# Kernel tuning notes

Hardware: AMD Instinct MI355X
Metric: run time of the kernel (lower is better)

Reference implementation:

```python
import jax, jax.numpy as jnp
import numpy as np

N_NODES = 50000
N_GRAPHS = 64


def gcn_conv(x, W, b, row, col, norm, n):
    # PyG GCNConv: h = x @ W; out[i] = sum_{(j,i) in E+selfloops} norm_ji * h[j] + b
    h = x @ W
    msg = norm[:, None] * h[row]
    out = jax.ops.segment_sum(msg, col, num_segments=n)
    return out + b


def setup_inputs() -> dict:
    key = jax.random.key(0)
    ks = jax.random.split(key, 12)
    F_in, H, C = 128, 128, 16
    x = jax.random.normal(ks[0], (N_NODES, F_in), dtype=jnp.float32)
    edge_index = jax.random.randint(ks[1], (2, 800000), 0, N_NODES, dtype=jnp.int64)
    batch = jnp.sort(jax.random.randint(ks[2], (N_NODES,), 0, N_GRAPHS, dtype=jnp.int64))
    def glorot(k, shape):
        lim = np.sqrt(6.0 / (shape[0] + shape[1]))
        return jax.random.uniform(k, shape, jnp.float32, -lim, lim)
    return {
        "x": x,
        "edge_index": edge_index,
        "batch": batch,
        "W0": glorot(ks[3], (F_in, H)), "b0": jnp.zeros((H,), jnp.float32),
        "W1": glorot(ks[4], (H, H)),   "b1": jnp.zeros((H,), jnp.float32),
        "W2": glorot(ks[5], (H, H)),   "b2": jnp.zeros((H,), jnp.float32),
        "lin_W": glorot(ks[6], (H, C)),
        "lin_b": jnp.zeros((C,), jnp.float32),
    }


def reference(x, edge_index, batch, W0, b0, W1, b1, W2, b2, lin_W, lin_b):
    n = x.shape[0]
    # add self-loops
    loops = jnp.arange(n, dtype=edge_index.dtype)
    row = jnp.concatenate([edge_index[0], loops])
    col = jnp.concatenate([edge_index[1], loops])
    # symmetric normalization: deg over destination (col) incl. self-loops
    deg = jax.ops.segment_sum(jnp.ones_like(col, dtype=x.dtype), col, num_segments=n)
    dinv = jnp.where(deg > 0, jax.lax.rsqrt(deg), 0.0)
    norm = dinv[row] * dinv[col]

    h = gcn_conv(x, W0, b0, row, col, norm, n)
    h = jax.nn.relu(h)
    h = gcn_conv(h, W1, b1, row, col, norm, n)
    h = jax.nn.relu(h)
    h = gcn_conv(h, W2, b2, row, col, norm, n)

    # global mean pool over graphs
    sums = jax.ops.segment_sum(h, batch, num_segments=N_GRAPHS)
    cnts = jax.ops.segment_sum(jnp.ones((n,), h.dtype), batch, num_segments=N_GRAPHS)
    pooled = sums / jnp.maximum(cnts, 1.0)[:, None]

    # dropout is identity in eval mode
    logits = pooled @ lin_W + lin_b
    return jax.nn.softmax(logits, axis=1)
```

## Files before the change

kernel.cpp:

```cpp
#include <hip/hip_runtime.h>


#define NF 128
#define MAXBUCK 512
#define CAP 2560
#define L1_CHUNK 8192
#define L1_THREADS 512
#define L1_PER_THREAD 16
#define PPG 8

typedef __attribute__((ext_vector_type(8))) short short8;
typedef __attribute__((ext_vector_type(4))) float floatx4;
typedef __attribute__((ext_vector_type(2))) float floatx2;

__device__ __forceinline__ unsigned int bf16_rne(float x) {
    unsigned int u = __float_as_uint(x);
    return (u + 0x7fffu + ((u >> 16) & 1u)) >> 16;
}
__device__ __forceinline__ unsigned int pack_bf16_rne(float x, float y) {
    return bf16_rne(x) | (bf16_rne(y) << 16);
}

__global__ __launch_bounds__(256) void k_repack_w3(const float* __restrict__ W0,
                                                   const float* __restrict__ W1,
                                                   const float* __restrict__ W2,
                                                   unsigned short* __restrict__ whi,
                                                   unsigned short* __restrict__ wlo,
                                                   int* __restrict__ bucket_cursor) {
    if (blockIdx.x == 0) {
        for (int i = threadIdx.x; i <= MAXBUCK; i += 256) bucket_cursor[i] = 0;
    }
    int wsel = blockIdx.x >> 3;
    const float* W = (wsel == 0) ? W0 : (wsel == 1) ? W1 : W2;
    int idx = (blockIdx.x & 7) * 256 + threadIdx.x;
    int slab = wsel * NF * NF;
    int l = idx & 63;
    int t = (idx >> 6) & 7;
    int s = idx >> 9;
    int kbase = s * 32 + (l >> 4) * 8;
    int nn = t * 16 + (l & 15);
    #pragma unroll
    for (int j = 0; j < 8; ++j) {
        float w = W[(kbase + j) * NF + nn];
        unsigned int h = bf16_rne(w);
        float hf = __uint_as_float(h << 16);
        unsigned int lo = bf16_rne(w - hf);
        whi[slab + idx * 8 + j] = (unsigned short)h;
        wlo[slab + idx * 8 + j] = (unsigned short)lo;
    }
}

__global__ __launch_bounds__(L1_THREADS) void k_bucket_scatter(
        const int* __restrict__ row, const int* __restrict__ colv,
        int* __restrict__ bucket_cursor, unsigned int* __restrict__ buck_arr,
        int ne, int etot, int nbuck) {
    __shared__ unsigned int hist[MAXBUCK];
    __shared__ unsigned int lbase[MAXBUCK];
    __shared__ unsigned int lcur[MAXBUCK];
    __shared__ unsigned int runb[MAXBUCK];
    __shared__ unsigned int sa[MAXBUCK], sb[MAXBUCK];
    __shared__ unsigned int reorder[L1_CHUNK];
    int t = threadIdx.x;
    int e0 = blockIdx.x * L1_CHUNK;
    int cnt_here = min(etot - e0, L1_CHUNK);

    hist[t] = 0;
    __syncthreads();

    unsigned int myv[L1_PER_THREAD];
    #pragma unroll
    for (int j = 0; j < L1_PER_THREAD; ++j) {
        int e = e0 + j * L1_THREADS + t;
        if (e < etot) {
            int s, d;
            if (e < ne) { s = row[e]; d = colv[e]; } else { s = d = e - ne; }
            myv[j] = (unsigned int)s | ((unsigned int)d << 16);
            atomicAdd(&hist[d >> 7], 1u);
        } else myv[j] = 0xffffffffu;
    }
    __syncthreads();

    sa[t] = hist[t];
    __syncthreads();
    unsigned int* pin = sa;
    unsigned int* pout = sb;
    #pragma unroll
    for (int off = 1; off < MAXBUCK; off <<= 1) {
        pout[t] = pin[t] + ((t >= off) ? pin[t - off] : 0);
        __syncthreads();
        unsigned int* tmp = pin; pin = pout; pout = tmp;
    }
    unsigned int ex = pin[t] - hist[t];
    lbase[t] = ex;
    lcur[t]  = ex;
    if (t < nbuck && hist[t] > 0)
        runb[t] = (unsigned int)atomicAdd(&bucket_cursor[t], (int)hist[t]);
    __syncthreads();

    #pragma unroll
    for (int j = 0; j < L1_PER_THREAD; ++j) {
        unsigned int v = myv[j];
        if (v != 0xffffffffu) {
            unsigned int p = atomicAdd(&lcur[v >> 23], 1u);
            reorder[p] = v;
        }
    }
    __syncthreads();

    for (int i = t; i < cnt_here; i += L1_THREADS) {
        unsigned int v = reorder[i];
        unsigned int b = v >> 23;
        buck_arr[(size_t)b * CAP + runb[b] + ((unsigned int)i - lbase[b])] = v;
    }
}

__global__ __launch_bounds__(256) void k_fine(const unsigned int* __restrict__ buck_arr,
                                              const int* __restrict__ bucket_cursor,
                                              int* __restrict__ starts,
                                              int* __restrict__ ends,
                                              float* __restrict__ dinv,
                                              unsigned short* __restrict__ src16,
                                              int n) {
    int b = blockIdx.x;
    int base = b * CAP;
    int m = min(bucket_cursor[b], CAP);
    int node0 = b << 7;
    int nn = min(128, n - node0);
    __shared__ unsigned int cnt[128];
    __shared__ unsigned int lsc[256];
    __shared__ unsigned int lcur[128];
    __shared__ unsigned short srcbuf[CAP];
    int t = threadIdx.x;
    if (t < 128) cnt[t] = 0;
    __syncthreads();
    for (int i = t; i < m; i += 256)
        atomicAdd(&cnt[(buck_arr[base + i] >> 16) - node0], 1u);
    __syncthreads();
    unsigned int v0 = (t < 128) ? cnt[t] : 0;
    lsc[t] = v0;
    __syncthreads();
    #pragma unroll
    for (int off = 1; off < 128; off <<= 1) {
        unsigned int add = (t >= off) ? lsc[t - off] : 0;
        __syncthreads();
        lsc[t] += add;
        __syncthreads();
    }
    if (t < 128) {
        unsigned int ex = lsc[t] - v0;
        lcur[t] = ex;
        if (t < nn) {
            starts[node0 + t] = base + (int)ex;
            ends[node0 + t]   = base + (int)(ex + v0);
            dinv[node0 + t]   = rsqrtf((float)v0);
        }
    }
    __syncthreads();
    for (int i = t; i < m; i += 256) {
        unsigned int v = buck_arr[base + i];
        unsigned int p = atomicAdd(&lcur[(v >> 16) - node0], 1u);
        srcbuf[p] = (unsigned short)(v & 0xffffu);
    }
    __syncthreads();
    for (int i = t; i < m; i += 256)
        src16[base + i] = srcbuf[i];
}

__global__ __launch_bounds__(256) void k_gemm_mfma(const float* __restrict__ Af,
                                                   const unsigned short* __restrict__ Ab,
                                                   const unsigned short* __restrict__ Whi,
                                                   const unsigned short* __restrict__ Wlo,
                                                   const float* __restrict__ dinv,
                                                   unsigned char* __restrict__ Out,
                                                   int M) {
    __shared__ unsigned short As[64 * 136];
    int tid = threadIdx.x;
    int row0 = blockIdx.x * 64;

    if (Af) {
        for (int c = tid; c < 1024; c += 256) {
            int r = c >> 4, off = c & 15;
            int gr = min(row0 + r, M - 1);
            const float4* p = (const float4*)(Af + (size_t)gr * NF) + off * 2;
            float4 v0 = p[0], v1 = p[1];
            uint4 pk;
            pk.x = pack_bf16_rne(v0.x, v0.y);
            pk.y = pack_bf16_rne(v0.z, v0.w);
            pk.z = pack_bf16_rne(v1.x, v1.y);
            pk.w = pack_bf16_rne(v1.z, v1.w);
            *(uint4*)(&As[r * 136 + off * 8]) = pk;
        }
    } else {
        for (int c = tid; c < 1024; c += 256) {
            int r = c >> 4, off = c & 15;
            int gr = min(row0 + r, M - 1);
            *(uint4*)(&As[r * 136 + off * 8]) = ((const uint4*)(Ab + (size_t)gr * NF))[off];
        }
    }
    __syncthreads();

    int wave = tid >> 6, l = tid & 63;
    int q = l >> 4, c16 = l & 15;
    int wrow0 = wave * 16;

    floatx4 acc[8];
    #pragma unroll
    for (int t = 0; t < 8; ++t) acc[t] = (floatx4){0.f, 0.f, 0.f, 0.f};

    #pragma unroll
    for (int s = 0; s < 4; ++s) {
        short8 a = *(const short8*)(&As[(wrow0 + c16) * 136 + s * 32 + q * 8]);
        #pragma unroll
        for (int t = 0; t < 8; ++t) {
            short8 bh = *(const short8*)(Whi + ((size_t)((s * 8 + t) * 64 + l) * 8));
            acc[t] = __builtin_amdgcn_mfma_f32_16x16x32_bf16(a, bh, acc[t], 0, 0, 0);
            short8 bl = *(const short8*)(Wlo + ((size_t)((s * 8 + t) * 64 + l) * 8));
            acc[t] = __builtin_amdgcn_mfma_f32_16x16x32_bf16(a, bl, acc[t], 0, 0, 0);
        }
    }

    float ds[4];
    #pragma unroll
    for (int i = 0; i < 4; ++i) {
        int gr = row0 + wrow0 + q * 4 + i;
        ds[i] = (gr < M) ? dinv[gr] : 0.f;
    }
    #pragma unroll
    for (int t = 0; t < 8; ++t) {
        #pragma unroll
        for (int i = 0; i < 4; ++i) {
            int gr = row0 + wrow0 + q * 4 + i;
            if (gr < M) {
                float v = acc[t][i] * ds[i];
                unsigned int pk = __builtin_amdgcn_cvt_pk_fp8_f32(v, v, 0, false);
                Out[(size_t)gr * NF + t * 16 + c16] = (unsigned char)(pk & 0xffu);
            }
        }
    }
}

__global__ __launch_bounds__(256) void k_agg_fp8(const unsigned char* __restrict__ hs8,
                                                 const int* __restrict__ starts,
                                                 const int* __restrict__ ends,
                                                 const unsigned short* __restrict__ src16,
                                                 const float* __restrict__ dinv,
                                                 const float* __restrict__ bias,
                                                 unsigned short* __restrict__ out,
                                                 int n, int do_relu) {
    int wave = threadIdx.x >> 6;
    int lane = threadIdx.x & 63;
    int node = blockIdx.x * 4 + wave;
    if (node >= n) return;
    int g = lane >> 4;
    int f = lane & 15;
    int start = starts[node], end = ends[node];

    const uint2* h2 = (const uint2*)hs8;
    float acc[8];
    #pragma unroll
    for (int j = 0; j < 8; ++j) acc[j] = 0.f;

    for (int base = start; base < end; base += 32) {
        int   sidx[8];
        float msk[8];
        #pragma unroll
        for (int j = 0; j < 8; ++j) {
            int e = base + g + 4 * j;
            bool v = e < end;
            sidx[j] = (int)src16[v ? e : start];
            msk[j]  = v ? 1.f : 0.f;
        }
        uint2 rr[8];
        #pragma unroll
        for (int j = 0; j < 8; ++j)
            rr[j] = h2[(size_t)sidx[j] * 16 + f];
        #pragma unroll
        for (int j = 0; j < 8; ++j) {
            float m = msk[j];
            floatx2 p0 = __builtin_amdgcn_cvt_pk_f32_fp8(rr[j].x, false);
            floatx2 p1 = __builtin_amdgcn_cvt_pk_f32_fp8(rr[j].x, true);
            floatx2 p2 = __builtin_amdgcn_cvt_pk_f32_fp8(rr[j].y, false);
            floatx2 p3 = __builtin_amdgcn_cvt_pk_f32_fp8(rr[j].y, true);
            acc[0] = fmaf(m, p0.x, acc[0]);
            acc[1] = fmaf(m, p0.y, acc[1]);
            acc[2] = fmaf(m, p1.x, acc[2]);
            acc[3] = fmaf(m, p1.y, acc[3]);
            acc[4] = fmaf(m, p2.x, acc[4]);
            acc[5] = fmaf(m, p2.y, acc[5]);
            acc[6] = fmaf(m, p3.x, acc[6]);
            acc[7] = fmaf(m, p3.y, acc[7]);
        }
    }

    #pragma unroll
    for (int j = 0; j < 8; ++j) {
        acc[j] += __shfl_xor(acc[j], 16);
        acc[j] += __shfl_xor(acc[j], 32);
    }

    if (g == 0) {
        float dd = dinv[node];
        float4 b0 = ((const float4*)bias)[2 * f];
        float4 b1 = ((const float4*)bias)[2 * f + 1];
        float r[8];
        r[0] = fmaf(dd, acc[0], b0.x); r[1] = fmaf(dd, acc[1], b0.y);
        r[2] = fmaf(dd, acc[2], b0.z); r[3] = fmaf(dd, acc[3], b0.w);
        r[4] = fmaf(dd, acc[4], b1.x); r[5] = fmaf(dd, acc[5], b1.y);
        r[6] = fmaf(dd, acc[6], b1.z); r[7] = fmaf(dd, acc[7], b1.w);
        if (do_relu) {
            #pragma unroll
            for (int j = 0; j < 8; ++j) r[j] = fmaxf(r[j], 0.f);
        }
        uint4 pk;
        pk.x = pack_bf16_rne(r[0], r[1]);
        pk.y = pack_bf16_rne(r[2], r[3]);
        pk.z = pack_bf16_rne(r[4], r[5]);
        pk.w = pack_bf16_rne(r[6], r[7]);
        ((uint4*)out)[(size_t)node * 16 + f] = pk;
    }
}

__global__ __launch_bounds__(128) void k_pool_partial(const unsigned short* __restrict__ h,
                                                      const int* __restrict__ batch,
                                                      float* __restrict__ pooled_part,
                                                      int n) {
    int b = blockIdx.x;
    int g = b / PPG;
    int j = b % PPG;
    int t = threadIdx.x;

    int lo = 0, hi = n;
    while (lo < hi) { int mid = (lo + hi) >> 1; if (batch[mid] < g) lo = mid + 1; else hi = mid; }
    int s = lo;
    lo = s; hi = n;
    while (lo < hi) { int mid = (lo + hi) >> 1; if (batch[mid] < g + 1) lo = mid + 1; else hi = mid; }
    int e = lo;

    int len = e - s;
    int chunk = (len + PPG - 1) / PPG;
    int i0 = s + j * chunk;
    int i1 = min(e, i0 + chunk);

    float acc = 0.f;
    for (int i = i0; i < i1; ++i)
        acc += __uint_as_float((unsigned int)h[(size_t)i * NF + t] << 16);
    pooled_part[(size_t)b * NF + t] = acc;
}

__global__ __launch_bounds__(1024) void k_head(const float* __restrict__ pooled_part,
                                               const int* __restrict__ batch,
                                               const float* __restrict__ linW,
                                               const float* __restrict__ linb,
                                               float* __restrict__ out,
                                               int n, int n_graphs) {
    __shared__ float ph[64 * NF];
    int t = threadIdx.x;
    for (int i = t; i < n_graphs * NF; i += 1024) {
        int g = i >> 7, f = i & 127;
        float s = 0.f;
        #pragma unroll
        for (int j = 0; j < PPG; ++j)
            s += pooled_part[(size_t)(g * PPG + j) * NF + f];
        ph[i] = s;
    }
    __syncthreads();

    int g = t >> 4;
    int c = t & 15;

    int lo = 0, hi = n;
    while (lo < hi) { int mid = (lo + hi) >> 1; if (batch[mid] < g) lo = mid + 1; else hi = mid; }
    int start = lo;
    lo = start; hi = n;
    while (lo < hi) { int mid = (lo + hi) >> 1; if (batch[mid] < g + 1) lo = mid + 1; else hi = mid; }
    float inv_cnt = 1.f / fmaxf((float)(lo - start), 1.f);

    float acc = linb[c];
    for (int k = 0; k < NF; ++k)
        acc += ph[g * NF + k] * inv_cnt * linW[k * 16 + c];

    float m = acc;
    #pragma unroll
    for (int s2 = 8; s2 >= 1; s2 >>= 1) m = fmaxf(m, __shfl_xor(m, s2, 16));
    float e = expf(acc - m);
    float ssum = e;
    #pragma unroll
    for (int s2 = 8; s2 >= 1; s2 >>= 1) ssum += __shfl_xor(ssum, s2, 16);
    out[g * 16 + c] = e / ssum;
}

extern "C" void kernel_launch(void* const* d_in, const int* in_sizes, int n_in,
                              void* d_out, int out_size, void* d_ws, size_t ws_size,
                              hipStream_t stream) {
    const float* x    = (const float*)d_in[0];
    const int*   edge = (const int*)d_in[1];
    const int*   batch= (const int*)d_in[2];
    const float* W0   = (const float*)d_in[3];
    const float* b0   = (const float*)d_in[4];
    const float* W1   = (const float*)d_in[5];
    const float* b1   = (const float*)d_in[6];
    const float* W2   = (const float*)d_in[7];
    const float* b2   = (const float*)d_in[8];
    const float* linW = (const float*)d_in[9];
    const float* linb = (const float*)d_in[10];

    int n  = in_sizes[0] / NF;
    int ne = in_sizes[1] / 2;
    int n_graphs = out_size / 16;
    const int* row  = edge;
    const int* colv = edge + ne;
    int etot = ne + n;
    int nbuck = (n + 127) >> 7;

    char* p = (char*)d_ws;
    auto alloc = [&](size_t bytes) { char* r = p; p += (bytes + 255) & ~(size_t)255; return r; };
    int*   bucket_cursor = (int*)alloc((size_t)(MAXBUCK + 1) * 4);
    unsigned int* buck_arr = (unsigned int*)alloc((size_t)MAXBUCK * CAP * 4);
    unsigned short* src16  = (unsigned short*)alloc((size_t)MAXBUCK * CAP * 2);
    int*   starts  = (int*)  alloc((size_t)n * 4);
    int*   ends    = (int*)  alloc((size_t)n * 4);
    float* dinv    = (float*)alloc((size_t)n * 4);
    unsigned char*  gbuf8 = (unsigned char*) alloc((size_t)n * NF);
    unsigned short* abuf  = (unsigned short*)alloc((size_t)n * NF * 2);
    float* pooled_part = (float*)alloc((size_t)n_graphs * PPG * NF * 4);
    unsigned short* whi = (unsigned short*)alloc((size_t)3 * NF * NF * 2);
    unsigned short* wlo = (unsigned short*)alloc((size_t)3 * NF * NF * 2);

    k_repack_w3<<<24, 256, 0, stream>>>(W0, W1, W2, whi, wlo, bucket_cursor);

    k_bucket_scatter<<<(etot + L1_CHUNK - 1) / L1_CHUNK, L1_THREADS, 0, stream>>>(
        row, colv, bucket_cursor, buck_arr, ne, etot, nbuck);
    k_fine<<<nbuck, 256, 0, stream>>>(buck_arr, bucket_cursor, starts, ends, dinv, src16, n);

    int gemm_blocks = (n + 63) / 64;
    int agg_blocks  = (n + 3) / 4;
    const size_t WSLAB = (size_t)NF * NF;

    k_gemm_mfma<<<gemm_blocks, 256, 0, stream>>>(x, nullptr, whi, wlo, dinv, gbuf8, n);
    k_agg_fp8  <<<agg_blocks, 256, 0, stream>>>(gbuf8, starts, ends, src16, dinv, b0, abuf, n, 1);
    k_gemm_mfma<<<gemm_blocks, 256, 0, stream>>>(nullptr, abuf, whi + WSLAB, wlo + WSLAB, dinv, gbuf8, n);
    k_agg_fp8  <<<agg_blocks, 256, 0, stream>>>(gbuf8, starts, ends, src16, dinv, b1, abuf, n, 1);
    k_gemm_mfma<<<gemm_blocks, 256, 0, stream>>>(nullptr, abuf, whi + 2 * WSLAB, wlo + 2 * WSLAB, dinv, gbuf8, n);
    k_agg_fp8  <<<agg_blocks, 256, 0, stream>>>(gbuf8, starts, ends, src16, dinv, b2, abuf, n, 0);

    k_pool_partial<<<n_graphs * PPG, 128, 0, stream>>>(abuf, batch, pooled_part, n);
    k_head<<<1, 1024, 0, stream>>>(pooled_part, batch, linW, linb, (float*)d_out, n, n_graphs);
}
```

Measured before the change: 292.3 us.

## Double GEMM row tile, vectorize pooling reads, halve bucket-scatter chunk size

```diff
diff --git a/kernel.cpp b/kernel.cpp
--- a/kernel.cpp
+++ b/kernel.cpp
@@ -4,9 +4,9 @@
 #define NF 128
 #define MAXBUCK 512
 #define CAP 2560
-#define L1_CHUNK 8192
+#define L1_CHUNK 4096
 #define L1_THREADS 512
-#define L1_PER_THREAD 16
+#define L1_PER_THREAD 8
 #define PPG 8
 
 typedef __attribute__((ext_vector_type(8))) short short8;
@@ -19,6 +19,9 @@
 }
 __device__ __forceinline__ unsigned int pack_bf16_rne(float x, float y) {
     return bf16_rne(x) | (bf16_rne(y) << 16);
+}
+__device__ __forceinline__ float bf16u_to_f32(unsigned int u) {
+    return __uint_as_float(u << 16);
 }
 
 __global__ __launch_bounds__(256) void k_repack_w3(const float* __restrict__ W0,
@@ -173,12 +176,12 @@
                                                    const float* __restrict__ dinv,
                                                    unsigned char* __restrict__ Out,
                                                    int M) {
-    __shared__ unsigned short As[64 * 136];
+    __shared__ unsigned short As[128 * 136];
     int tid = threadIdx.x;
-    int row0 = blockIdx.x * 64;
+    int row0 = blockIdx.x * 128;
 
     if (Af) {
-        for (int c = tid; c < 1024; c += 256) {
+        for (int c = tid; c < 2048; c += 256) {
             int r = c >> 4, off = c & 15;
             int gr = min(row0 + r, M - 1);
             const float4* p = (const float4*)(Af + (size_t)gr * NF) + off * 2;
@@ -191,7 +194,7 @@
             *(uint4*)(&As[r * 136 + off * 8]) = pk;
         }
     } else {
-        for (int c = tid; c < 1024; c += 256) {
+        for (int c = tid; c < 2048; c += 256) {
             int r = c >> 4, off = c & 15;
             int gr = min(row0 + r, M - 1);
             *(uint4*)(&As[r * 136 + off * 8]) = ((const uint4*)(Ab + (size_t)gr * NF))[off];
@@ -203,37 +206,45 @@
     int q = l >> 4, c16 = l & 15;
     int wrow0 = wave * 16;
 
-    floatx4 acc[8];
-    #pragma unroll
-    for (int t = 0; t < 8; ++t) acc[t] = (floatx4){0.f, 0.f, 0.f, 0.f};
+    floatx4 acc[2][8];
+    #pragma unroll
+    for (int h = 0; h < 2; ++h)
+        #pragma unroll
+        for (int t = 0; t < 8; ++t) acc[h][t] = (floatx4){0.f, 0.f, 0.f, 0.f};
 
     #pragma unroll
     for (int s = 0; s < 4; ++s) {
-        short8 a = *(const short8*)(&As[(wrow0 + c16) * 136 + s * 32 + q * 8]);
+        short8 a0 = *(const short8*)(&As[(wrow0 + c16) * 136 + s * 32 + q * 8]);
+        short8 a1 = *(const short8*)(&As[(64 + wrow0 + c16) * 136 + s * 32 + q * 8]);
         #pragma unroll
         for (int t = 0; t < 8; ++t) {
             short8 bh = *(const short8*)(Whi + ((size_t)((s * 8 + t) * 64 + l) * 8));
-            acc[t] = __builtin_amdgcn_mfma_f32_16x16x32_bf16(a, bh, acc[t], 0, 0, 0);
             short8 bl = *(const short8*)(Wlo + ((size_t)((s * 8 + t) * 64 + l) * 8));
-            acc[t] = __builtin_amdgcn_mfma_f32_16x16x32_bf16(a, bl, acc[t], 0, 0, 0);
-        }
-    }
-
-    float ds[4];
-    #pragma unroll
-    for (int i = 0; i < 4; ++i) {
-        int gr = row0 + wrow0 + q * 4 + i;
-        ds[i] = (gr < M) ? dinv[gr] : 0.f;
-    }
-    #pragma unroll
-    for (int t = 0; t < 8; ++t) {
+            acc[0][t] = __builtin_amdgcn_mfma_f32_16x16x32_bf16(a0, bh, acc[0][t], 0, 0, 0);
+            acc[0][t] = __builtin_amdgcn_mfma_f32_16x16x32_bf16(a0, bl, acc[0][t], 0, 0, 0);
+            acc[1][t] = __builtin_amdgcn_mfma_f32_16x16x32_bf16(a1, bh, acc[1][t], 0, 0, 0);
+            acc[1][t] = __builtin_amdgcn_mfma_f32_16x16x32_bf16(a1, bl, acc[1][t], 0, 0, 0);
+        }
+    }
+
+    #pragma unroll
+    for (int h = 0; h < 2; ++h) {
+        float ds[4];
         #pragma unroll
         for (int i = 0; i < 4; ++i) {
-            int gr = row0 + wrow0 + q * 4 + i;
-            if (gr < M) {
-                float v = acc[t][i] * ds[i];
-                unsigned int pk = __builtin_amdgcn_cvt_pk_fp8_f32(v, v, 0, false);
-                Out[(size_t)gr * NF + t * 16 + c16] = (unsigned char)(pk & 0xffu);
+            int gr = row0 + h * 64 + wrow0 + q * 4 + i;
+            ds[i] = (gr < M) ? dinv[gr] : 0.f;
+        }
+        #pragma unroll
+        for (int t = 0; t < 8; ++t) {
+            #pragma unroll
+            for (int i = 0; i < 4; ++i) {
+                int gr = row0 + h * 64 + wrow0 + q * 4 + i;
+                if (gr < M) {
+                    float v = acc[h][t][i] * ds[i];
+                    unsigned int pk = __builtin_amdgcn_cvt_pk_fp8_f32(v, v, 0, false);
+                    Out[(size_t)gr * NF + t * 16 + c16] = (unsigned char)(pk & 0xffu);
+                }
             }
         }
     }
@@ -324,6 +335,7 @@
                                                       const int* __restrict__ batch,
                                                       float* __restrict__ pooled_part,
                                                       int n) {
+    __shared__ float red[8][NF];
     int b = blockIdx.x;
     int g = b / PPG;
     int j = b % PPG;
@@ -341,10 +353,24 @@
     int i0 = s + j * chunk;
     int i1 = min(e, i0 + chunk);
 
-    float acc = 0.f;
-    for (int i = i0; i < i1; ++i)
-        acc += __uint_as_float((unsigned int)h[(size_t)i * NF + t] << 16);
-    pooled_part[(size_t)b * NF + t] = acc;
+    int r = t >> 4, f8 = t & 15;
+    float acc[8];
+    #pragma unroll
+    for (int k = 0; k < 8; ++k) acc[k] = 0.f;
+    for (int i = i0 + r; i < i1; i += 8) {
+        uint4 v = *(const uint4*)(&h[(size_t)i * NF + f8 * 8]);
+        acc[0] += bf16u_to_f32(v.x & 0xffffu); acc[1] += bf16u_to_f32(v.x >> 16);
+        acc[2] += bf16u_to_f32(v.y & 0xffffu); acc[3] += bf16u_to_f32(v.y >> 16);
+        acc[4] += bf16u_to_f32(v.z & 0xffffu); acc[5] += bf16u_to_f32(v.z >> 16);
+        acc[6] += bf16u_to_f32(v.w & 0xffffu); acc[7] += bf16u_to_f32(v.w >> 16);
+    }
+    #pragma unroll
+    for (int k = 0; k < 8; ++k) red[r][f8 * 8 + k] = acc[k];
+    __syncthreads();
+    float ssum = 0.f;
+    #pragma unroll
+    for (int rr = 0; rr < 8; ++rr) ssum += red[rr][t];
+    pooled_part[(size_t)b * NF + t] = ssum;
 }
 
 __global__ __launch_bounds__(1024) void k_head(const float* __restrict__ pooled_part,
@@ -432,7 +458,7 @@
         row, colv, bucket_cursor, buck_arr, ne, etot, nbuck);
     k_fine<<<nbuck, 256, 0, stream>>>(buck_arr, bucket_cursor, starts, ends, dinv, src16, n);
 
-    int gemm_blocks = (n + 63) / 64;
+    int gemm_blocks = (n + 127) / 128;
     int agg_blocks  = (n + 3) / 4;
     const size_t WSLAB = (size_t)NF * NF;
 
```

Result: faster. 277.2 us (-5.2%).
